# Kernel tuning notes

Measured on AMD Instinct MI355X. Metric: run time of the kernel, lower is better.

Reference implementation:

```python
import jax, jax.numpy as jnp
import numpy as np

H = 12
D_K = 64
NEG = -1e9
EPS = 1e-6
SQRT_2_PI = float(np.sqrt(2.0 / np.pi))


def gelu_tanh(x):
    return 0.5 * x * (1.0 + jnp.tanh(SQRT_2_PI * (x + 0.044715 * x * x * x)))


def layernorm(x, a, b):
    # torch std is unbiased (ddof=1); note original adds eps to std, not var
    mean = jnp.mean(x, axis=-1, keepdims=True)
    n = x.shape[-1]
    var = jnp.sum((x - mean) ** 2, axis=-1, keepdims=True) / (n - 1)
    std = jnp.sqrt(var)
    return a * (x - mean) / (std + EPS) + b


def setup_inputs() -> dict:
    key = jax.random.key(0)
    ks = jax.random.split(key, 16)
    B, S, D, F = 8, 1024, 768, 3072
    s = 0.02
    inp = {
        "x": jax.random.normal(ks[0], (B, S, D), jnp.float32),
        "mask": jnp.ones((B, 1, 1, S), jnp.int32),
        "Wq": jax.random.normal(ks[1], (D, D), jnp.float32) * s,
        "bq": jnp.zeros((D,), jnp.float32),
        "Wk": jax.random.normal(ks[2], (D, D), jnp.float32) * s,
        "bk": jnp.zeros((D,), jnp.float32),
        "Wv": jax.random.normal(ks[3], (D, D), jnp.float32) * s,
        "bv": jnp.zeros((D,), jnp.float32),
        "Wo": jax.random.normal(ks[4], (D, D), jnp.float32) * s,
        "bo": jnp.zeros((D,), jnp.float32),
        "W1": jax.random.normal(ks[5], (D, F), jnp.float32) * s,
        "b1": jnp.zeros((F,), jnp.float32),
        "W2": jax.random.normal(ks[6], (F, D), jnp.float32) * s,
        "b2": jnp.zeros((D,), jnp.float32),
        "ln1_a": jnp.ones((D,), jnp.float32),
        "ln1_b": jnp.ones((D,), jnp.float32),
        "ln2_a": jnp.ones((D,), jnp.float32),
        "ln2_b": jnp.ones((D,), jnp.float32),
    }
    return inp


def reference(x, mask, Wq, bq, Wk, bk, Wv, bv, Wo, bo, W1, b1, W2, b2,
              ln1_a, ln1_b, ln2_a, ln2_b):
    B, S, D = x.shape
    # QKV projections -> [B, H, S, d_k]
    def split_heads(t):
        return t.reshape(B, S, H, D_K).transpose(0, 2, 1, 3)
    q = split_heads(x @ Wq + bq)
    k = split_heads(x @ Wk + bk)
    v = split_heads(x @ Wv + bv)
    scores = jnp.einsum("bhqd,bhkd->bhqk", q, k) / jnp.sqrt(jnp.float32(D_K))
    scores = jnp.where(mask == 0, jnp.float32(NEG), scores)
    p = jax.nn.softmax(scores, axis=-1)
    attn = jnp.einsum("bhqk,bhkd->bhqd", p, v)
    attn = attn.transpose(0, 2, 1, 3).reshape(B, S, D)
    attn_out = attn @ Wo + bo
    out1 = layernorm(x + attn_out, ln1_a, ln1_b)
    ffn = gelu_tanh(out1 @ W1 + b1) @ W2 + b2
    out2 = layernorm(out1 + ffn, ln2_a, ln2_b)
    return out2
```

## Files before the change

kernel.cpp:

```cpp
#include <hip/hip_runtime.h>
#include <hip/hip_bf16.h>
#include <math.h>

#define BB 8
#define SS 1024
#define DD 768
#define FF 3072
#define HH 12
#define DK 64

typedef __bf16 bf16;
typedef __attribute__((ext_vector_type(8))) __bf16 bf16x8;
typedef __attribute__((ext_vector_type(4))) __bf16 bf16x4;
typedef __attribute__((ext_vector_type(4))) float f32x4;

#define AS1 __attribute__((address_space(1)))
#define AS3 __attribute__((address_space(3)))

#define EXP2_SCALE 0.18033688011112042f
#define NLOG2E2    -2.8853900817779268f
#define MASK_BIAS  -1.8033688e8f

__device__ __forceinline__ float gelu_fast(float x) {
    const float u = 0.7978845608028654f * (x + 0.044715f * x * x * x);
    const float e = __builtin_amdgcn_exp2f(u * NLOG2E2);
    return x * __builtin_amdgcn_rcpf(1.0f + e);
}

template<int BN, int OUTB, int GELU_F, int RESID, int VT, int RB16>
__global__ __launch_bounds__(256) void gemm_bf16(
    const bf16* __restrict__ A, const bf16* __restrict__ Bt,
    const float* __restrict__ bias, const void* __restrict__ R,
    void* __restrict__ Cout, bf16* __restrict__ Vt, int M, int N, int K)
{
    constexpr int NTJ   = BN / 32;
    constexpr int BITER = (BN * 8) / 256;

    __shared__ bf16x8 As[1024];
    __shared__ bf16x8 Bs[BN * 8];

    const int t    = threadIdx.x;
    const int wave = t >> 6;
    const int lane = t & 63;
    const int mtiles = M >> 7;
    const int m0 = (blockIdx.x % mtiles) * 128;
    const int n0 = (blockIdx.x / mtiles) * BN;
    const int wm = (wave >> 1) * 64;
    const int wn = (wave & 1) * (BN / 2);
    const int col  = lane & 15;
    const int quad = lane >> 4;

    f32x4 acc[4][NTJ] = {};

    const bf16* Abase = A  + (size_t)m0 * K;
    const bf16* Bbase = Bt + (size_t)n0 * K;

    for (int k0 = 0; k0 < K; k0 += 64) {
        if (k0) __syncthreads();

        #pragma unroll
        for (int i = 0; i < 4; ++i) {
            const int chunk = i * 256 + wave * 64 + lane;
            const int r  = chunk >> 3;
            const int kc = (chunk & 7) ^ (r & 7);
            const bf16* ga = Abase + (size_t)r * K + k0 + kc * 8;
            __builtin_amdgcn_global_load_lds((AS1 void*)ga, (AS3 void*)(As + i * 256 + wave * 64), 16, 0, 0);
        }
        #pragma unroll
        for (int i = 0; i < BITER; ++i) {
            const int chunk = i * 256 + wave * 64 + lane;
            const int r  = chunk >> 3;
            const int kc = (chunk & 7) ^ (r & 7);
            const bf16* gb = Bbase + (size_t)r * K + k0 + kc * 8;
            __builtin_amdgcn_global_load_lds((AS1 void*)gb, (AS3 void*)(Bs + i * 256 + wave * 64), 16, 0, 0);
        }
        __syncthreads();

        const bf16* Asp = (const bf16*)As;
        const bf16* Bsp = (const bf16*)Bs;
        #pragma unroll
        for (int ks = 0; ks < 2; ++ks) {
            bf16x8 af[4], bfr[NTJ];
            #pragma unroll
            for (int ti = 0; ti < 4; ++ti) {
                const int r  = wm + ti * 16 + col;
                const int cs = (ks * 4 + quad) ^ (r & 7);
                af[ti] = *(const bf16x8*)(Asp + r * 64 + cs * 8);
            }
            #pragma unroll
            for (int tj = 0; tj < NTJ; ++tj) {
                const int r  = wn + tj * 16 + col;
                const int cs = (ks * 4 + quad) ^ (r & 7);
                bfr[tj] = *(const bf16x8*)(Bsp + r * 64 + cs * 8);
            }
            #pragma unroll
            for (int ti = 0; ti < 4; ++ti)
                #pragma unroll
                for (int tj = 0; tj < NTJ; ++tj)
                    acc[ti][tj] = __builtin_amdgcn_mfma_f32_16x16x32_bf16(
                        af[ti], bfr[tj], acc[ti][tj], 0, 0, 0);
        }
    }

    float biasv[NTJ];
    #pragma unroll
    for (int tj = 0; tj < NTJ; ++tj) biasv[tj] = bias[n0 + wn + tj * 16 + col];

    #pragma unroll
    for (int ti = 0; ti < 4; ++ti) {
        #pragma unroll
        for (int tj = 0; tj < NTJ; ++tj) {
            const int n = n0 + wn + tj * 16 + col;
            const bool vcol = VT && (n >= 2 * DD);
            if (VT && vcol) {
                const int hh = (n - 2 * DD) >> 6;
                const int dd = (n - 2 * DD) & 63;
                const int mb = m0 + wm + ti * 16 + quad * 4;
                const int bb = mb >> 10, ss0 = mb & 1023;
                bf16x4 pk;
                #pragma unroll
                for (int i = 0; i < 4; ++i)
                    pk[i] = (bf16)(acc[ti][tj][i] + biasv[tj]);
                *(bf16x4*)(Vt + (size_t)((bb * HH + hh) * DK + dd) * SS + ss0) = pk;
            } else {
                #pragma unroll
                for (int i = 0; i < 4; ++i) {
                    const int m = m0 + wm + ti * 16 + quad * 4 + i;
                    float v = acc[ti][tj][i] + biasv[tj];
                    if (GELU_F) v = gelu_fast(v);
                    if (RESID) {
                        if (RB16) v += (float)((const bf16*)R)[(size_t)m * N + n];
                        else      v += ((const float*)R)[(size_t)m * N + n];
                    }
                    if (OUTB) ((bf16*)Cout)[(size_t)m * N + n] = (bf16)v;
                    else      ((float*)Cout)[(size_t)m * N + n] = v;
                }
            }
        }
    }
}

__device__ __forceinline__ void tc32(
    const float* __restrict__ src, bf16* __restrict__ dst,
    int R, int C, int c0, int r0, int t)
{
    __shared__ float tile[32][33];
    const int tx = t & 31, ty = t >> 5;
    #pragma unroll
    for (int i = 0; i < 32; i += 8)
        tile[ty + i][tx] = src[(size_t)(r0 + ty + i) * C + c0 + tx];
    __syncthreads();
    #pragma unroll
    for (int i = 0; i < 32; i += 8)
        dst[(size_t)(c0 + ty + i) * R + r0 + tx] = (bf16)tile[tx][ty + i];
}

__global__ __launch_bounds__(256) void prep_all(
    const float* __restrict__ Wq, const float* __restrict__ Wk,
    const float* __restrict__ Wv, const float* __restrict__ Wo,
    const float* __restrict__ W1, const float* __restrict__ W2,
    const float* __restrict__ bq, const float* __restrict__ bk,
    const float* __restrict__ bv, const float* __restrict__ x,
    bf16* __restrict__ wqkvb, bf16* __restrict__ wob,
    bf16* __restrict__ wt1b,  bf16* __restrict__ wt2b,
    float* __restrict__ bqkv, bf16x4* __restrict__ xb)
{
    const int blk = blockIdx.x;
    const int t = threadIdx.x;
    if (blk < 2304) {
        const int job = blk / 576, loc = blk % 576;
        const int c0 = (loc % 24) * 32, r0 = (loc / 24) * 32;
        const float* src = (job == 0) ? Wq : (job == 1) ? Wk : (job == 2) ? Wv : Wo;
        bf16* dst = (job == 3) ? wob : wqkvb + (size_t)job * DD * DD;
        tc32(src, dst, DD, DD, c0, r0, t);
    } else if (blk < 4608) {
        const int loc = blk - 2304;
        tc32(W1, wt1b, DD, FF, (loc % 96) * 32, (loc / 96) * 32, t);
    } else if (blk < 6912) {
        const int loc = blk - 4608;
        tc32(W2, wt2b, FF, DD, (loc % 24) * 32, (loc / 24) * 32, t);
    } else if (blk < 6921) {
        const int i = (blk - 6912) * 256 + t;
        if (i < 3 * DD)
            bqkv[i] = (i < DD) ? bq[i] : (i < 2 * DD ? bk[i - DD] : bv[i - 2 * DD]);
    } else {
        const int i = (blk - 6921) * 256 + t;
        const float4 v = ((const float4*)x)[i];
        bf16x4 o;
        o.x = (bf16)v.x; o.y = (bf16)v.y; o.z = (bf16)v.z; o.w = (bf16)v.w;
        xb[i] = o;
    }
}

__global__ __launch_bounds__(256) void flash_mfma(
    const bf16* __restrict__ qkvb,
    const bf16* __restrict__ vtb,
    const int*  __restrict__ mask,
    bf16* __restrict__ O)
{
    __shared__ bf16x8 Ks[512];
    __shared__ bf16x8 Vs[512];
    __shared__ bf16   Ps[4 * 32 * 64];
    __shared__ float  Mb[SS];

    const int t    = threadIdx.x;
    const int wave = t >> 6;
    const int lane = t & 63;
    const int col  = lane & 15;
    const int quad = lane >> 4;
    const int bh = blockIdx.x % (BB * HH);
    const int q0 = (blockIdx.x / (BB * HH)) * 128;
    const int b  = bh / HH;
    const int h  = bh % HH;

    #pragma unroll
    for (int i = 0; i < 4; ++i) {
        const int c = t + i * 256;
        Mb[c] = (mask[b * SS + c] == 0) ? MASK_BIAS : 0.0f;
    }

    bf16x8 aq[2][2];
    #pragma unroll
    for (int mi = 0; mi < 2; ++mi)
        #pragma unroll
        for (int ks = 0; ks < 2; ++ks)
            aq[mi][ks] = *(const bf16x8*)(qkvb
                + (size_t)(b * SS + q0 + wave * 32 + mi * 16 + col) * 2304
                + h * DK + ks * 32 + quad * 8);

    f32x4 o[2][4] = {};
    float l_part[2][4] = {};

    bf16* Pw = Ps + wave * 2048;

    for (int c0 = 0; c0 < SS; c0 += 64) {
        if (c0) __syncthreads();

        #pragma unroll
        for (int i = 0; i < 2; ++i) {
            const int s  = i * 256 + wave * 64 + lane;
            const int r  = s >> 3;
            const int kc = (s & 7) ^ (r & 7);
            const bf16* gk = qkvb + (size_t)(b * SS + c0 + r) * 2304 + DD + h * DK + kc * 8;
            __builtin_amdgcn_global_load_lds((AS1 void*)gk, (AS3 void*)(Ks + i * 256 + wave * 64), 16, 0, 0);
            const bf16* gv = vtb + (size_t)(bh * DK + r) * SS + c0 + kc * 8;
            __builtin_amdgcn_global_load_lds((AS1 void*)gv, (AS3 void*)(Vs + i * 256 + wave * 64), 16, 0, 0);
        }
        __syncthreads();

        const bf16* Ksp = (const bf16*)Ks;
        f32x4 s4[2][4] = {};
        {
            bf16x8 kf[2][4];
            #pragma unroll
            for (int ks = 0; ks < 2; ++ks)
                #pragma unroll
                for (int tj = 0; tj < 4; ++tj) {
                    const int r  = tj * 16 + col;
                    const int sl = (ks * 4 + quad) ^ (r & 7);
                    kf[ks][tj] = *(const bf16x8*)(Ksp + r * 64 + sl * 8);
                }
            #pragma unroll
            for (int mi = 0; mi < 2; ++mi)
                #pragma unroll
                for (int ks = 0; ks < 2; ++ks)
                    #pragma unroll
                    for (int tj = 0; tj < 4; ++tj)
                        s4[mi][tj] = __builtin_amdgcn_mfma_f32_16x16x32_bf16(
                            aq[mi][ks], kf[ks][tj], s4[mi][tj], 0, 0, 0);
        }

        float mbv[4];
        #pragma unroll
        for (int tj = 0; tj < 4; ++tj) mbv[tj] = Mb[c0 + tj * 16 + col];

        #pragma unroll
        for (int mi = 0; mi < 2; ++mi)
            #pragma unroll
            for (int i = 0; i < 4; ++i) {
                const int rf = mi * 16 + quad * 4 + i;
                #pragma unroll
                for (int tj = 0; tj < 4; ++tj) {
                    const float p = __builtin_amdgcn_exp2f(
                        __builtin_fmaf(s4[mi][tj][i], EXP2_SCALE, mbv[tj]));
                    l_part[mi][i] += p;
                    const int c  = tj * 16 + col;
                    const int sl = ((c >> 3) ^ (rf & 7));
                    Pw[rf * 64 + sl * 8 + (c & 7)] = (bf16)p;
                }
            }

        const bf16* Vsp = (const bf16*)Vs;
        bf16x8 vf[2][4];
        #pragma unroll
        for (int ks = 0; ks < 2; ++ks)
            #pragma unroll
            for (int tj = 0; tj < 4; ++tj) {
                const int r  = tj * 16 + col;
                const int sl = (ks * 4 + quad) ^ (r & 7);
                vf[ks][tj] = *(const bf16x8*)(Vsp + r * 64 + sl * 8);
            }
        #pragma unroll
        for (int mi = 0; mi < 2; ++mi) {
            bf16x8 pf[2];
            #pragma unroll
            for (int ks = 0; ks < 2; ++ks) {
                const int rf = mi * 16 + col;
                const int sl = (ks * 4 + quad) ^ (rf & 7);
                pf[ks] = *(const bf16x8*)(Pw + rf * 64 + sl * 8);
            }
            #pragma unroll
            for (int ks = 0; ks < 2; ++ks)
                #pragma unroll
                for (int tj = 0; tj < 4; ++tj)
                    o[mi][tj] = __builtin_amdgcn_mfma_f32_16x16x32_bf16(
                        pf[ks], vf[ks][tj], o[mi][tj], 0, 0, 0);
        }
    }

    #pragma unroll
    for (int mi = 0; mi < 2; ++mi)
        #pragma unroll
        for (int i = 0; i < 4; ++i) {
            float l = l_part[mi][i];
            #pragma unroll
            for (int off = 1; off < 16; off <<= 1)
                l += __shfl_xor(l, off, 64);
            const float inv = 1.0f / l;
            const int q = q0 + wave * 32 + mi * 16 + quad * 4 + i;
            #pragma unroll
            for (int tj = 0; tj < 4; ++tj)
                O[(size_t)(b * SS + q) * DD + h * DK + tj * 16 + col] =
                    (bf16)(o[mi][tj][i] * inv);
        }
}

template<int IN_B16, int OUTF, int OUTBF>
__global__ __launch_bounds__(256) void layernorm_k(
    const void* __restrict__ X,
    const float* __restrict__ ga, const float* __restrict__ gb,
    float* __restrict__ out, bf16* __restrict__ outb)
{
    __shared__ float red[4];
    const int row = blockIdx.x;
    const int t   = threadIdx.x;

    float v[3];
    #pragma unroll
    for (int i = 0; i < 3; ++i) {
        const int c = t + i * 256;
        if (IN_B16) v[i] = (float)((const bf16*)X)[(size_t)row * DD + c];
        else        v[i] = ((const float*)X)[(size_t)row * DD + c];
    }

    float s = v[0] + v[1] + v[2];
    #pragma unroll
    for (int off = 32; off > 0; off >>= 1) s += __shfl_down(s, off, 64);
    if ((t & 63) == 0) red[t >> 6] = s;
    __syncthreads();
    const float mean = (red[0] + red[1] + red[2] + red[3]) * (1.0f / 768.0f);
    __syncthreads();

    float sq = 0.f;
    #pragma unroll
    for (int i = 0; i < 3; ++i) { const float d = v[i] - mean; sq += d * d; }
    #pragma unroll
    for (int off = 32; off > 0; off >>= 1) sq += __shfl_down(sq, off, 64);
    if ((t & 63) == 0) red[t >> 6] = sq;
    __syncthreads();
    const float var = (red[0] + red[1] + red[2] + red[3]) * (1.0f / 767.0f);
    const float inv = 1.0f / (sqrtf(var) + 1e-6f);

    #pragma unroll
    for (int i = 0; i < 3; ++i) {
        const int c = t + i * 256;
        const float r = ga[c] * (v[i] - mean) * inv + gb[c];
        if (OUTF)  out[(size_t)row * DD + c] = r;
        if (OUTBF) outb[(size_t)row * DD + c] = (bf16)r;
    }
}

extern "C" void kernel_launch(void* const* d_in, const int* in_sizes, int n_in,
                              void* d_out, int out_size, void* d_ws, size_t ws_size,
                              hipStream_t stream)
{
    const float* x    = (const float*)d_in[0];
    const int*   mask = (const int*)  d_in[1];
    const float* Wq   = (const float*)d_in[2];
    const float* bq   = (const float*)d_in[3];
    const float* Wk   = (const float*)d_in[4];
    const float* bk   = (const float*)d_in[5];
    const float* Wv   = (const float*)d_in[6];
    const float* bv   = (const float*)d_in[7];
    const float* Wo   = (const float*)d_in[8];
    const float* bo   = (const float*)d_in[9];
    const float* W1   = (const float*)d_in[10];
    const float* b1   = (const float*)d_in[11];
    const float* W2   = (const float*)d_in[12];
    const float* b2   = (const float*)d_in[13];
    const float* ln1a = (const float*)d_in[14];
    const float* ln1b = (const float*)d_in[15];
    const float* ln2a = (const float*)d_in[16];
    const float* ln2b = (const float*)d_in[17];
    float* out = (float*)d_out;

    const int M = BB * SS;
    const size_t nBSD = (size_t)M * DD;

    char* w = (char*)d_ws;
    bf16*  qkvb  = (bf16*)w;            w += (size_t)M * 3 * DD * 2;
    bf16*  vtb   = (bf16*)w;            w += (size_t)BB * HH * DK * SS * 2;
    bf16*  attnb = (bf16*)w;            w += nBSD * 2;
    bf16*  attn_sum = (bf16*)w;         w += nBSD * 2;
    bf16*  ffn_sum = (bf16*)w;          w += nBSD * 2;
    bf16*  xb    = (bf16*)w;            w += nBSD * 2;
    bf16*  hbuf  = (bf16*)w;            w += (size_t)M * FF * 2;
    bf16*  wqkvb = (bf16*)w;            w += (size_t)3 * DD * DD * 2;
    bf16*  wob   = (bf16*)w;            w += (size_t)DD * DD * 2;
    bf16*  wt1b  = (bf16*)w;            w += (size_t)DD * FF * 2;
    bf16*  wt2b  = (bf16*)w;            w += (size_t)FF * DD * 2;
    float* bqkv  = (float*)w;           w += (size_t)3 * DD * 4;
    bf16*  out1b = xb;

    const dim3 blk(256);

    prep_all<<<dim3(13065), blk, 0, stream>>>(
        Wq, Wk, Wv, Wo, W1, W2, bq, bk, bv, x,
        wqkvb, wob, wt1b, wt2b, bqkv, (bf16x4*)xb);

    gemm_bf16<128, 1, 0, 0, 1, 0><<<dim3((M / 128) * (3 * DD / 128)), blk, 0, stream>>>(
        xb, wqkvb, bqkv, nullptr, qkvb, vtb, M, 3 * DD, DD);

    flash_mfma<<<dim3((SS / 128) * BB * HH), blk, 0, stream>>>(qkvb, vtb, mask, attnb);

    gemm_bf16<64, 1, 0, 1, 0, 1><<<dim3((M / 128) * (DD / 64)), blk, 0, stream>>>(
        attnb, wob, bo, xb, attn_sum, nullptr, M, DD, DD);

    layernorm_k<1, 0, 1><<<dim3(M), blk, 0, stream>>>(
        attn_sum, ln1a, ln1b, nullptr, out1b);

    gemm_bf16<128, 1, 1, 0, 0, 0><<<dim3((M / 128) * (FF / 128)), blk, 0, stream>>>(
        out1b, wt1b, b1, nullptr, hbuf, nullptr, M, FF, DD);

    gemm_bf16<64, 1, 0, 1, 0, 1><<<dim3((M / 128) * (DD / 64)), blk, 0, stream>>>(
        hbuf, wt2b, b2, out1b, ffn_sum, nullptr, M, DD, FF);

    layernorm_k<1, 1, 0><<<dim3(M), blk, 0, stream>>>(
        ffn_sum, ln2a, ln2b, out, nullptr);
}
```

Baseline: 364.5 us.

## Split flash attention block into 8 waves of 16 query rows each

The attention kernel moves from 4 waves handling 32 query rows each to 8 waves handling 16 rows each, so each block now runs 512 threads over the same 128-row query tile. Each thread issues one K and one V async LDS load per chunk instead of two. Per-wave register use drops because the Q fragments, scores and output accumulators shrink by half, which could raise occupancy and latency hiding. In exchange, each K/V fragment read from LDS feeds half as many MFMAs, so LDS read traffic per unit of math doubles, and barriers now synchronise twice as many waves.

```diff
diff --git a/kernel.cpp b/kernel.cpp
--- a/kernel.cpp
+++ b/kernel.cpp
@@ -192,7 +192,7 @@
     }
 }
 
-__global__ __launch_bounds__(256) void flash_mfma(
+__global__ __launch_bounds__(512) void flash_mfma(
     const bf16* __restrict__ qkvb,
     const bf16* __restrict__ vtb,
     const int*  __restrict__ mask,
@@ -200,7 +200,7 @@
 {
     __shared__ bf16x8 Ks[512];
     __shared__ bf16x8 Vs[512];
-    __shared__ bf16   Ps[4 * 32 * 64];
+    __shared__ bf16   Ps[8 * 16 * 64];
     __shared__ float  Mb[SS];
 
     const int t    = threadIdx.x;
@@ -214,42 +214,38 @@
     const int h  = bh % HH;
 
     #pragma unroll
-    for (int i = 0; i < 4; ++i) {
-        const int c = t + i * 256;
+    for (int i = 0; i < 2; ++i) {
+        const int c = t + i * 512;
         Mb[c] = (mask[b * SS + c] == 0) ? MASK_BIAS : 0.0f;
     }
 
-    bf16x8 aq[2][2];
-    #pragma unroll
-    for (int mi = 0; mi < 2; ++mi)
-        #pragma unroll
-        for (int ks = 0; ks < 2; ++ks)
-            aq[mi][ks] = *(const bf16x8*)(qkvb
-                + (size_t)(b * SS + q0 + wave * 32 + mi * 16 + col) * 2304
-                + h * DK + ks * 32 + quad * 8);
-
-    f32x4 o[2][4] = {};
-    float l_part[2][4] = {};
-
-    bf16* Pw = Ps + wave * 2048;
+    bf16x8 aq[2];
+    #pragma unroll
+    for (int ks = 0; ks < 2; ++ks)
+        aq[ks] = *(const bf16x8*)(qkvb
+            + (size_t)(b * SS + q0 + wave * 16 + col) * 2304
+            + h * DK + ks * 32 + quad * 8);
+
+    f32x4 o[4] = {};
+    float l_part[4] = {};
+
+    bf16* Pw = Ps + wave * 1024;
 
     for (int c0 = 0; c0 < SS; c0 += 64) {
         if (c0) __syncthreads();
 
-        #pragma unroll
-        for (int i = 0; i < 2; ++i) {
-            const int s  = i * 256 + wave * 64 + lane;
-            const int r  = s >> 3;
-            const int kc = (s & 7) ^ (r & 7);
+        {
+            const int r  = t >> 3;
+            const int kc = (t & 7) ^ (r & 7);
             const bf16* gk = qkvb + (size_t)(b * SS + c0 + r) * 2304 + DD + h * DK + kc * 8;
-            __builtin_amdgcn_global_load_lds((AS1 void*)gk, (AS3 void*)(Ks + i * 256 + wave * 64), 16, 0, 0);
+            __builtin_amdgcn_global_load_lds((AS1 void*)gk, (AS3 void*)(Ks + t), 16, 0, 0);
             const bf16* gv = vtb + (size_t)(bh * DK + r) * SS + c0 + kc * 8;
-            __builtin_amdgcn_global_load_lds((AS1 void*)gv, (AS3 void*)(Vs + i * 256 + wave * 64), 16, 0, 0);
+            __builtin_amdgcn_global_load_lds((AS1 void*)gv, (AS3 void*)(Vs + t), 16, 0, 0);
         }
         __syncthreads();
 
         const bf16* Ksp = (const bf16*)Ks;
-        f32x4 s4[2][4] = {};
+        f32x4 s4[4] = {};
         {
             bf16x8 kf[2][4];
             #pragma unroll
@@ -261,13 +257,11 @@
                     kf[ks][tj] = *(const bf16x8*)(Ksp + r * 64 + sl * 8);
                 }
             #pragma unroll
-            for (int mi = 0; mi < 2; ++mi)
-                #pragma unroll
-                for (int ks = 0; ks < 2; ++ks)
-                    #pragma unroll
-                    for (int tj = 0; tj < 4; ++tj)
-                        s4[mi][tj] = __builtin_amdgcn_mfma_f32_16x16x32_bf16(
-                            aq[mi][ks], kf[ks][tj], s4[mi][tj], 0, 0, 0);
+            for (int ks = 0; ks < 2; ++ks)
+                #pragma unroll
+                for (int tj = 0; tj < 4; ++tj)
+                    s4[tj] = __builtin_amdgcn_mfma_f32_16x16x32_bf16(
+                        aq[ks], kf[ks][tj], s4[tj], 0, 0, 0);
         }
 
         float mbv[4];
@@ -275,20 +269,18 @@
         for (int tj = 0; tj < 4; ++tj) mbv[tj] = Mb[c0 + tj * 16 + col];
 
         #pragma unroll
-        for (int mi = 0; mi < 2; ++mi)
-            #pragma unroll
-            for (int i = 0; i < 4; ++i) {
-                const int rf = mi * 16 + quad * 4 + i;
-                #pragma unroll
-                for (int tj = 0; tj < 4; ++tj) {
-                    const float p = __builtin_amdgcn_exp2f(
-                        __builtin_fmaf(s4[mi][tj][i], EXP2_SCALE, mbv[tj]));
-                    l_part[mi][i] += p;
-                    const int c  = tj * 16 + col;
-                    const int sl = ((c >> 3) ^ (rf & 7));
-                    Pw[rf * 64 + sl * 8 + (c & 7)] = (bf16)p;
-                }
-            }
+        for (int i = 0; i < 4; ++i) {
+            const int rf = quad * 4 + i;
+            #pragma unroll
+            for (int tj = 0; tj < 4; ++tj) {
+                const float p = __builtin_amdgcn_exp2f(
+                    __builtin_fmaf(s4[tj][i], EXP2_SCALE, mbv[tj]));
+                l_part[i] += p;
+                const int c  = tj * 16 + col;
+                const int sl = ((c >> 3) ^ (rf & 7));
+                Pw[rf * 64 + sl * 8 + (c & 7)] = (bf16)p;
+            }
+        }
 
         const bf16* Vsp = (const bf16*)Vs;
         bf16x8 vf[2][4];
@@ -300,12 +292,11 @@
                 const int sl = (ks * 4 + quad) ^ (r & 7);
                 vf[ks][tj] = *(const bf16x8*)(Vsp + r * 64 + sl * 8);
             }
-        #pragma unroll
-        for (int mi = 0; mi < 2; ++mi) {
+        {
             bf16x8 pf[2];
             #pragma unroll
             for (int ks = 0; ks < 2; ++ks) {
-                const int rf = mi * 16 + col;
+                const int rf = col;
                 const int sl = (ks * 4 + quad) ^ (rf & 7);
                 pf[ks] = *(const bf16x8*)(Pw + rf * 64 + sl * 8);
             }
@@ -313,26 +304,24 @@
             for (int ks = 0; ks < 2; ++ks)
                 #pragma unroll
                 for (int tj = 0; tj < 4; ++tj)
-                    o[mi][tj] = __builtin_amdgcn_mfma_f32_16x16x32_bf16(
-                        pf[ks], vf[ks][tj], o[mi][tj], 0, 0, 0);
-        }
-    }
-
-    #pragma unroll
-    for (int mi = 0; mi < 2; ++mi)
-        #pragma unroll
-        for (int i = 0; i < 4; ++i) {
-            float l = l_part[mi][i];
-            #pragma unroll
-            for (int off = 1; off < 16; off <<= 1)
-                l += __shfl_xor(l, off, 64);
-            const float inv = 1.0f / l;
-            const int q = q0 + wave * 32 + mi * 16 + quad * 4 + i;
-            #pragma unroll
-            for (int tj = 0; tj < 4; ++tj)
-                O[(size_t)(b * SS + q) * DD + h * DK + tj * 16 + col] =
-                    (bf16)(o[mi][tj][i] * inv);
-        }
+                    o[tj] = __builtin_amdgcn_mfma_f32_16x16x32_bf16(
+                        pf[ks], vf[ks][tj], o[tj], 0, 0, 0);
+        }
+    }
+
+    #pragma unroll
+    for (int i = 0; i < 4; ++i) {
+        float l = l_part[i];
+        #pragma unroll
+        for (int off = 1; off < 16; off <<= 1)
+            l += __shfl_xor(l, off, 64);
+        const float inv = 1.0f / l;
+        const int q = q0 + wave * 16 + quad * 4 + i;
+        #pragma unroll
+        for (int tj = 0; tj < 4; ++tj)
+            O[(size_t)(b * SS + q) * DD + h * DK + tj * 16 + col] =
+                (bf16)(o[tj][i] * inv);
+    }
 }
 
 template<int IN_B16, int OUTF, int OUTBF>
@@ -431,7 +420,8 @@
     gemm_bf16<128, 1, 0, 0, 1, 0><<<dim3((M / 128) * (3 * DD / 128)), blk, 0, stream>>>(
         xb, wqkvb, bqkv, nullptr, qkvb, vtb, M, 3 * DD, DD);
 
-    flash_mfma<<<dim3((SS / 128) * BB * HH), blk, 0, stream>>>(qkvb, vtb, mask, attnb);
+    flash_mfma<<<dim3((SS / 128) * BB * HH), dim3(512), 0, stream>>>(
+        qkvb, vtb, mask, attnb);
 
     gemm_bf16<64, 1, 0, 1, 0, 1><<<dim3((M / 128) * (DD / 64)), blk, 0, stream>>>(
         attnb, wob, bo, xb, attn_sum, nullptr, M, DD, DD);
```

After: 352.7 us. 3.2% less time.
